# Performance work log

Measured on AMD Instinct MI355X. Metric: run time of the kernel, lower is better.

The kernel has to match this reference:

```python
import jax, jax.numpy as jnp
import numpy as np

N_NODES = 50000
N_EDGES = 400000
D = 512
LN_EPS = 1e-5


def setup_inputs() -> dict:
    key = jax.random.key(0)
    k0, k1, k2, k3 = jax.random.split(key, 4)
    x = jax.random.normal(k0, (N_NODES, D), dtype=jnp.float32)
    src = jax.random.randint(k1, (N_EDGES,), 0, N_NODES, dtype=jnp.int64)
    dst = jax.random.randint(k2, (N_EDGES,), 0, N_NODES, dtype=jnp.int64)
    W = jax.random.normal(k3, (D, D), dtype=jnp.float32) * 0.05
    b = jnp.zeros((D,), dtype=jnp.float32)
    gamma = jnp.ones((D,), dtype=jnp.float32)
    beta = jnp.zeros((D,), dtype=jnp.float32)
    return {"x": x, "W": W, "b": b, "gamma": gamma, "beta": beta, "src": src, "dst": dst}


def reference(x, W, b, gamma, beta, src, dst):
    n = x.shape[0]
    ones = jnp.ones(src.shape, dtype=x.dtype)
    # DGL GraphConv norm='both': clamp degrees to >= 1
    deg_out = jnp.clip(jax.ops.segment_sum(ones, src, num_segments=n), 1.0)  # [N]
    deg_in = jnp.clip(jax.ops.segment_sum(ones, dst, num_segments=n), 1.0)   # [N]
    h = x * jax.lax.rsqrt(deg_out)[:, None]                 # [N, D] src normalization
    agg = jax.ops.segment_sum(h[src], dst, num_segments=n)  # gather->scatter-add SpMM
    h = agg * jax.lax.rsqrt(deg_in)[:, None]                # dst normalization
    h = h @ W + b                                           # dense linear
    # LayerNorm over last dim
    mu = jnp.mean(h, axis=-1, keepdims=True)
    var = jnp.mean(jnp.square(h - mu), axis=-1, keepdims=True)
    h = (h - mu) * jax.lax.rsqrt(var + LN_EPS) * gamma + beta
    # torch nn.GELU default = exact erf GELU
    return jax.nn.gelu(h, approximate=False)
```

## Files before the change

kernel.cpp:

```cpp
#include <hip/hip_runtime.h>
#include <hip/hip_bf16.h>

#define D 512

typedef __attribute__((ext_vector_type(8))) short bf16x8;
typedef __attribute__((ext_vector_type(4))) float f32x4;

__device__ inline float b2f(short h) {
    union { unsigned u; float f; } c;
    c.u = ((unsigned)(unsigned short)h) << 16;
    return c.f;
}

__global__ void k_hist(const int* __restrict__ src, const int* __restrict__ dst,
                       int* __restrict__ deg_out, int* __restrict__ deg_in, int E) {
    int e = blockIdx.x * 256 + threadIdx.x;
    if (e < E) {
        atomicAdd(&deg_out[src[e]], 1);
        atomicAdd(&deg_in[dst[e]], 1);
    }
}

__global__ __launch_bounds__(256)
void k_scale(const float* __restrict__ x, const int* __restrict__ deg_out,
             __hip_bfloat16* __restrict__ xs, int total16) {
    int i = blockIdx.x * 256 + threadIdx.x;
    if (i >= total16) return;
    int node = i >> 6;
    float w = rsqrtf((float)max(deg_out[node], 1));
    const float4* p = (const float4*)(x + (size_t)i * 8);
    float4 a = p[0], b = p[1];
    union { float4 f4; __hip_bfloat16 h[8]; } o;
    o.h[0] = __float2bfloat16(a.x * w);
    o.h[1] = __float2bfloat16(a.y * w);
    o.h[2] = __float2bfloat16(a.z * w);
    o.h[3] = __float2bfloat16(a.w * w);
    o.h[4] = __float2bfloat16(b.x * w);
    o.h[5] = __float2bfloat16(b.y * w);
    o.h[6] = __float2bfloat16(b.z * w);
    o.h[7] = __float2bfloat16(b.w * w);
    *(float4*)(xs + (size_t)i * 8) = o.f4;
}

__global__ void k_scan1(const int* __restrict__ deg_in, int* __restrict__ row_start,
                        int* __restrict__ partials, int N) {
    __shared__ int sm[1024];
    int tid = threadIdx.x;
    int i = blockIdx.x * 1024 + tid;
    int v = (i < N) ? deg_in[i] : 0;
    sm[tid] = v;
    __syncthreads();
    int acc = v;
    #pragma unroll
    for (int off = 1; off < 1024; off <<= 1) {
        int t = (tid >= off) ? sm[tid - off] : 0;
        __syncthreads();
        acc += t;
        sm[tid] = acc;
        __syncthreads();
    }
    if (i < N) row_start[i] = acc - v;
    if (tid == 1023) partials[blockIdx.x] = acc;
}

__global__ void k_scan2w(int* __restrict__ partials, int* __restrict__ row_start,
                         int nb, int N) {
    int lane = threadIdx.x;
    int orig = (lane < nb) ? partials[lane] : 0;
    int v = orig;
    #pragma unroll
    for (int off = 1; off < 64; off <<= 1) {
        int t = __shfl_up(v, off, 64);
        if (lane >= off) v += t;
    }
    if (lane < nb) partials[lane] = v - orig;
    if (lane == 63) row_start[N] = v;
}

__global__ void k_scan2s(int* __restrict__ partials, int* __restrict__ row_start,
                         int nb, int N) {
    if (threadIdx.x == 0 && blockIdx.x == 0) {
        int run = 0;
        for (int b = 0; b < nb; b++) { int t = partials[b]; partials[b] = run; run += t; }
        row_start[N] = run;
    }
}

__global__ void k_scan3(int* __restrict__ row_start, const int* __restrict__ partials, int N) {
    int i = blockIdx.x * 256 + threadIdx.x;
    if (i < N) row_start[i] += partials[i >> 10];
}

__global__ void k_fill(const int* __restrict__ src, const int* __restrict__ dst,
                       const int* __restrict__ row_start, int* __restrict__ cursor,
                       int* __restrict__ csr_src, int E) {
    int e = blockIdx.x * 256 + threadIdx.x;
    if (e < E) {
        int d = dst[e];
        int slot = atomicAdd(&cursor[d], 1);
        csr_src[row_start[d] + slot] = src[e];
    }
}

__global__ void k_packw2(const float* __restrict__ W, __hip_bfloat16* __restrict__ Wp) {
    int bid = blockIdx.x;
    int c = bid >> 7, kt = (bid >> 3) & 15, ntc = bid & 7;
    int lane = threadIdx.x;
    int k0 = kt * 32 + (lane >> 4) * 8;
    int n  = (c * 8 + ntc) * 16 + (lane & 15);
    union { float4 f4; __hip_bfloat16 h[8]; } o;
    #pragma unroll
    for (int j = 0; j < 8; j++)
        o.h[j] = __float2bfloat16(W[(size_t)(k0 + j) * D + n]);
    *(float4*)(Wp + ((size_t)bid * 64 + lane) * 8) = o.f4;
}

__global__ __launch_bounds__(512, 2)
void k_fused(const __hip_bfloat16* __restrict__ xs, const int* __restrict__ row_start,
             const int* __restrict__ csr_src, const __hip_bfloat16* __restrict__ Wp,
             const float* __restrict__ bias, const float* __restrict__ gamma,
             const float* __restrict__ beta, float* __restrict__ out, int M) {
    __shared__ __align__(16) char ldsA[65536];
    __shared__ float s_sum[64][4];
    __shared__ float s_sq[64][4];

    int tid = threadIdx.x;
    int wid = tid >> 6, lane = tid & 63;
    int l4 = lane >> 4, coll = lane & 15;
    int tb = blockIdx.x * 64;

    {
        const __hip_bfloat16* xl = xs + (size_t)lane * 8;
        for (int i = 0; i < 8; i++) {
            int rowt = wid * 8 + i;
            int node = tb + rowt;
            char* dst = ldsA + rowt * 1024 + ((lane * 16) ^ ((rowt & 7) << 4));
            if (node < M) {
                int rs = row_start[node], re = row_start[node + 1];
                float acc[8];
                #pragma unroll
                for (int k = 0; k < 8; k++) acc[k] = 0.f;
                int j = rs;
                for (; j + 4 <= re; j += 4) {
                    int s0 = csr_src[j], s1 = csr_src[j + 1], s2 = csr_src[j + 2], s3 = csr_src[j + 3];
                    bf16x8 v0 = *(const bf16x8*)(xl + (size_t)s0 * D);
                    bf16x8 v1 = *(const bf16x8*)(xl + (size_t)s1 * D);
                    bf16x8 v2 = *(const bf16x8*)(xl + (size_t)s2 * D);
                    bf16x8 v3 = *(const bf16x8*)(xl + (size_t)s3 * D);
                    #pragma unroll
                    for (int k = 0; k < 8; k++)
                        acc[k] += (b2f(v0[k]) + b2f(v1[k])) + (b2f(v2[k]) + b2f(v3[k]));
                }
                for (; j < re; j++) {
                    int s = csr_src[j];
                    bf16x8 v = *(const bf16x8*)(xl + (size_t)s * D);
                    #pragma unroll
                    for (int k = 0; k < 8; k++) acc[k] += b2f(v[k]);
                }
                float rn = rsqrtf((float)max(re - rs, 1));
                union { float4 f4; __hip_bfloat16 h[8]; } o;
                #pragma unroll
                for (int k = 0; k < 8; k++) o.h[k] = __float2bfloat16(acc[k] * rn);
                *(float4*)dst = o.f4;
            } else {
                *(float4*)dst = (float4){0.f, 0.f, 0.f, 0.f};
            }
        }
    }
    __syncthreads();

    int wm = wid >> 2, wn = wid & 3;
    int r0 = wm * 32 + coll;
    int r1 = r0 + 16;
    const char* wb = (const char*)Wp + ((size_t)(wn * 128) * 64 + lane) * 16;

    f32x4 acc0[8], acc1[8];
    #pragma unroll
    for (int t = 0; t < 8; t++) { acc0[t] = (f32x4){0,0,0,0}; acc1[t] = (f32x4){0,0,0,0}; }

    for (int kt = 0; kt < 16; kt++) {
        int kb = kt * 64 + l4 * 16;
        bf16x8 af0 = *(const bf16x8*)(ldsA + r0 * 1024 + (kb ^ ((r0 & 7) << 4)));
        bf16x8 af1 = *(const bf16x8*)(ldsA + r1 * 1024 + (kb ^ ((r1 & 7) << 4)));
        const char* wk = wb + (size_t)kt * 8192;
        #pragma unroll
        for (int t = 0; t < 8; t++) {
            bf16x8 bf = *(const bf16x8*)(wk + (size_t)t * 1024);
            acc0[t] = __builtin_amdgcn_mfma_f32_16x16x32_bf16(af0, bf, acc0[t], 0, 0, 0);
            acc1[t] = __builtin_amdgcn_mfma_f32_16x16x32_bf16(af1, bf, acc1[t], 0, 0, 0);
        }
    }

    float bia[8], gam[8], bet[8];
    #pragma unroll
    for (int t = 0; t < 8; t++) {
        int col = wn * 128 + t * 16 + coll;
        bia[t] = bias[col]; gam[t] = gamma[col]; bet[t] = beta[col];
    }
    #pragma unroll
    for (int ai = 0; ai < 2; ai++) {
        f32x4* acc = ai ? acc1 : acc0;
        #pragma unroll
        for (int r = 0; r < 4; r++) {
            float s = 0.f, q = 0.f;
            #pragma unroll
            for (int t = 0; t < 8; t++) {
                float v = acc[t][r] + bia[t];
                acc[t][r] = v;
                s += v; q += v * v;
            }
            #pragma unroll
            for (int off = 1; off < 16; off <<= 1) {
                s += __shfl_xor(s, off, 64);
                q += __shfl_xor(q, off, 64);
            }
            if (coll == 0) {
                int rb = wm * 32 + ai * 16 + l4 * 4 + r;
                s_sum[rb][wn] = s;
                s_sq[rb][wn] = q;
            }
        }
    }
    __syncthreads();

    #pragma unroll
    for (int ai = 0; ai < 2; ai++) {
        f32x4* acc = ai ? acc1 : acc0;
        #pragma unroll
        for (int r = 0; r < 4; r++) {
            int rb = wm * 32 + ai * 16 + l4 * 4 + r;
            int gr = tb + rb;
            if (gr >= M) continue;
            float s = s_sum[rb][0] + s_sum[rb][1] + s_sum[rb][2] + s_sum[rb][3];
            float q = s_sq[rb][0] + s_sq[rb][1] + s_sq[rb][2] + s_sq[rb][3];
            float mean = s * (1.0f / 512.0f);
            float var = q * (1.0f / 512.0f) - mean * mean;
            float rstd = rsqrtf(fmaxf(var, 0.f) + 1e-5f);
            float* orow = out + (size_t)gr * D + wn * 128 + coll;
            #pragma unroll
            for (int t = 0; t < 8; t++) {
                float y = (acc[t][r] - mean) * rstd * gam[t] + bet[t];
                float yy = y * y;
                float pz = fmaf(yy, -0.1029423374f, -2.3022076728f);
                float e = __builtin_amdgcn_exp2f(y * pz);
                float g = y * __builtin_amdgcn_rcpf(1.0f + e);
                orow[t * 16] = g;
            }
        }
    }
}

__global__ __launch_bounds__(256)
void k_spmm_f32(const float* __restrict__ x, const int* __restrict__ row_start,
                const int* __restrict__ csr_src, const int* __restrict__ deg_out,
                __hip_bfloat16* __restrict__ A, int N) {
    int wid = threadIdx.x >> 6;
    int lane = threadIdx.x & 63;
    int node = blockIdx.x * 4 + wid;
    if (node >= N) return;
    int rs = row_start[node], re = row_start[node + 1];
    float4 acc0 = {0.f, 0.f, 0.f, 0.f};
    float4 acc1 = {0.f, 0.f, 0.f, 0.f};
    const float* xl = x + (size_t)lane * 8;
    for (int j = rs; j < re; j++) {
        int s = csr_src[j];
        float w = rsqrtf((float)max(deg_out[s], 1));
        const float4* p = (const float4*)(xl + (size_t)s * D);
        float4 a = p[0], b = p[1];
        acc0.x += a.x * w; acc0.y += a.y * w; acc0.z += a.z * w; acc0.w += a.w * w;
        acc1.x += b.x * w; acc1.y += b.y * w; acc1.z += b.z * w; acc1.w += b.w * w;
    }
    float rn = rsqrtf((float)max(re - rs, 1));
    union { float4 f4; __hip_bfloat16 h[8]; } o;
    o.h[0] = __float2bfloat16(acc0.x * rn);
    o.h[1] = __float2bfloat16(acc0.y * rn);
    o.h[2] = __float2bfloat16(acc0.z * rn);
    o.h[3] = __float2bfloat16(acc0.w * rn);
    o.h[4] = __float2bfloat16(acc1.x * rn);
    o.h[5] = __float2bfloat16(acc1.y * rn);
    o.h[6] = __float2bfloat16(acc1.z * rn);
    o.h[7] = __float2bfloat16(acc1.w * rn);
    *(float4*)(A + (size_t)node * D + lane * 8) = o.f4;
}

__global__ void k_packw(const float* __restrict__ W, __hip_bfloat16* __restrict__ Wp) {
    int tile = blockIdx.x;
    int lane = threadIdx.x;
    int kt = tile >> 5, nt = tile & 31;
    int k0 = kt * 32 + (lane >> 4) * 8;
    int n  = nt * 16 + (lane & 15);
    union { float4 f4; __hip_bfloat16 h[8]; } o;
    #pragma unroll
    for (int j = 0; j < 8; j++)
        o.h[j] = __float2bfloat16(W[(size_t)(k0 + j) * D + n]);
    *(float4*)(Wp + ((size_t)tile * 64 + lane) * 8) = o.f4;
}

__global__ __launch_bounds__(512)
void k_gemm(const __hip_bfloat16* __restrict__ A, const __hip_bfloat16* __restrict__ Wp,
            const float* __restrict__ bias, const float* __restrict__ gamma,
            const float* __restrict__ beta, float* __restrict__ out, int M) {
    int tid = threadIdx.x;
    int wid = tid >> 6, lane = tid & 63;
    int wm = wid >> 2;
    int wn = wid & 3;
    int l4 = lane >> 4, coll = lane & 15;
    int m0 = blockIdx.x * 32 + wm * 16;
    int arow = m0 + coll;
    bool rowok = (arow < M);

    f32x4 acc[8];
    #pragma unroll
    for (int t = 0; t < 8; t++) acc[t] = (f32x4){0.f, 0.f, 0.f, 0.f};

    const bf16x8* wpb = (const bf16x8*)Wp;
    for (int kt = 0; kt < 16; kt++) {
        bf16x8 afrag;
        if (rowok) afrag = *(const bf16x8*)(A + (size_t)arow * D + kt * 32 + l4 * 8);
        else afrag = (bf16x8){0,0,0,0,0,0,0,0};
        const bf16x8* wp = wpb + ((size_t)(kt * 32 + wn * 8) * 64 + lane);
        #pragma unroll
        for (int t = 0; t < 8; t++) {
            bf16x8 bfrag = wp[(size_t)t * 64];
            acc[t] = __builtin_amdgcn_mfma_f32_16x16x32_bf16(afrag, bfrag, acc[t], 0, 0, 0);
        }
    }
    __shared__ float s_sum[32][4];
    __shared__ float s_sq[32][4];
    #pragma unroll
    for (int r = 0; r < 4; r++) {
        float s = 0.f, q = 0.f;
        #pragma unroll
        for (int t = 0; t < 8; t++) {
            int col = wn * 128 + t * 16 + coll;
            float v = acc[t][r] + bias[col];
            acc[t][r] = v;
            s += v; q += v * v;
        }
        #pragma unroll
        for (int off = 1; off < 16; off <<= 1) {
            s += __shfl_xor(s, off, 64);
            q += __shfl_xor(q, off, 64);
        }
        if (coll == 0) {
            int rb = wm * 16 + l4 * 4 + r;
            s_sum[rb][wn] = s;
            s_sq[rb][wn] = q;
        }
    }
    __syncthreads();
    #pragma unroll
    for (int r = 0; r < 4; r++) {
        int rb = wm * 16 + l4 * 4 + r;
        int gr = blockIdx.x * 32 + rb;
        if (gr >= M) continue;
        float s = s_sum[rb][0] + s_sum[rb][1] + s_sum[rb][2] + s_sum[rb][3];
        float q = s_sq[rb][0] + s_sq[rb][1] + s_sq[rb][2] + s_sq[rb][3];
        float mean = s * (1.0f / 512.0f);
        float var = q * (1.0f / 512.0f) - mean * mean;
        float rstd = rsqrtf(fmaxf(var, 0.f) + 1e-5f);
        #pragma unroll
        for (int t = 0; t < 8; t++) {
            int col = wn * 128 + t * 16 + coll;
            float y = (acc[t][r] - mean) * rstd * gamma[col] + beta[col];
            float yy = y * y;
            float pz = fmaf(yy, -0.1029423374f, -2.3022076728f);
            float e = __builtin_amdgcn_exp2f(y * pz);
            out[(size_t)gr * D + col] = y * __builtin_amdgcn_rcpf(1.0f + e);
        }
    }
}

extern "C" void kernel_launch(void* const* d_in, const int* in_sizes, int n_in,
                              void* d_out, int out_size, void* d_ws, size_t ws_size,
                              hipStream_t stream) {
    const float* x     = (const float*)d_in[0];
    const float* W     = (const float*)d_in[1];
    const float* b     = (const float*)d_in[2];
    const float* gamma = (const float*)d_in[3];
    const float* beta  = (const float*)d_in[4];
    const int*   src   = (const int*)d_in[5];
    const int*   dst   = (const int*)d_in[6];
    int N = in_sizes[0] / D;
    int E = in_sizes[5];
    float* out = (float*)d_out;

    int* deg_out   = (int*)d_ws;
    int* deg_in    = deg_out + N;
    int* row_start = deg_in + N;
    int* cursor    = row_start + N + 1;
    int* partials  = cursor + N;
    int* csr_src   = partials + 64;
    uintptr_t p = (uintptr_t)(csr_src + E);
    p = (p + 255) & ~(uintptr_t)255;
    __hip_bfloat16* A = (__hip_bfloat16*)p;
    p += (size_t)N * D * sizeof(__hip_bfloat16);
    p = (p + 255) & ~(uintptr_t)255;
    __hip_bfloat16* Wp = (__hip_bfloat16*)p;
    p += (size_t)D * D * sizeof(__hip_bfloat16);
    p = (p + 255) & ~(uintptr_t)255;
    __hip_bfloat16* xs = (__hip_bfloat16*)p;
    size_t need_xs = (p - (uintptr_t)d_ws) + (size_t)N * D * sizeof(__hip_bfloat16);
    bool use_bf16_path = (ws_size >= need_xs);

    hipMemsetAsync(deg_out, 0, (size_t)2 * N * sizeof(int), stream);
    hipMemsetAsync(cursor, 0, (size_t)N * sizeof(int), stream);

    k_hist<<<(E + 255) / 256, 256, 0, stream>>>(src, dst, deg_out, deg_in, E);
    int nb1 = (N + 1023) / 1024;
    k_scan1<<<nb1, 1024, 0, stream>>>(deg_in, row_start, partials, N);
    if (nb1 <= 64)
        k_scan2w<<<1, 64, 0, stream>>>(partials, row_start, nb1, N);
    else
        k_scan2s<<<1, 64, 0, stream>>>(partials, row_start, nb1, N);
    k_scan3<<<(N + 255) / 256, 256, 0, stream>>>(row_start, partials, N);
    k_fill<<<(E + 255) / 256, 256, 0, stream>>>(src, dst, row_start, cursor, csr_src, E);

    if (use_bf16_path) {
        int total16 = N * 64;
        k_scale<<<(total16 + 255) / 256, 256, 0, stream>>>(x, deg_out, xs, total16);
        k_packw2<<<512, 64, 0, stream>>>(W, Wp);
        k_fused<<<(N + 63) / 64, 512, 0, stream>>>(xs, row_start, csr_src, Wp,
                                                   b, gamma, beta, out, N);
    } else {
        k_spmm_f32<<<(N + 3) / 4, 256, 0, stream>>>(x, row_start, csr_src, deg_out, A, N);
        k_packw<<<512, 64, 0, stream>>>(W, Wp);
        k_gemm<<<(N + 31) / 32, 512, 0, stream>>>(A, Wp, b, gamma, beta, out, N);
    }
}
```

Measured before the change: 291.4 us.

## Reorder to GEMM-then-aggregate: compute x·W first, gather transformed rows with fused LayerNorm/GELU

Uses linearity to apply the dense matmul before the sparse aggregation. A new GEMM kernel reads fp32 x directly, converts it to bf16 in registers, scales rows by the src-degree norm and writes a bf16 Y buffer. A gather kernel then sums neighbour rows of Y, applies the dst norm, bias, LayerNorm and GELU in one wave per node. This drops the separate scaling pass and the xs buffer, and takes the sparse gather out of the GEMM kernel, where it made the MFMA phase wait. In exchange the GEMM result is rounded to bf16 before aggregation and makes an extra round trip through memory.

```diff
diff --git a/kernel.cpp b/kernel.cpp
--- a/kernel.cpp
+++ b/kernel.cpp
@@ -19,27 +19,6 @@
         atomicAdd(&deg_out[src[e]], 1);
         atomicAdd(&deg_in[dst[e]], 1);
     }
-}
-
-__global__ __launch_bounds__(256)
-void k_scale(const float* __restrict__ x, const int* __restrict__ deg_out,
-             __hip_bfloat16* __restrict__ xs, int total16) {
-    int i = blockIdx.x * 256 + threadIdx.x;
-    if (i >= total16) return;
-    int node = i >> 6;
-    float w = rsqrtf((float)max(deg_out[node], 1));
-    const float4* p = (const float4*)(x + (size_t)i * 8);
-    float4 a = p[0], b = p[1];
-    union { float4 f4; __hip_bfloat16 h[8]; } o;
-    o.h[0] = __float2bfloat16(a.x * w);
-    o.h[1] = __float2bfloat16(a.y * w);
-    o.h[2] = __float2bfloat16(a.z * w);
-    o.h[3] = __float2bfloat16(a.w * w);
-    o.h[4] = __float2bfloat16(b.x * w);
-    o.h[5] = __float2bfloat16(b.y * w);
-    o.h[6] = __float2bfloat16(b.z * w);
-    o.h[7] = __float2bfloat16(b.w * w);
-    *(float4*)(xs + (size_t)i * 8) = o.f4;
 }
 
 __global__ void k_scan1(const int* __restrict__ deg_in, int* __restrict__ row_start,
@@ -116,62 +95,22 @@
 }
 
 __global__ __launch_bounds__(512, 2)
-void k_fused(const __hip_bfloat16* __restrict__ xs, const int* __restrict__ row_start,
-             const int* __restrict__ csr_src, const __hip_bfloat16* __restrict__ Wp,
-             const float* __restrict__ bias, const float* __restrict__ gamma,
-             const float* __restrict__ beta, float* __restrict__ out, int M) {
-    __shared__ __align__(16) char ldsA[65536];
-    __shared__ float s_sum[64][4];
-    __shared__ float s_sq[64][4];
+void k_gemmY(const float* __restrict__ x, const __hip_bfloat16* __restrict__ Wp,
+             const int* __restrict__ deg_out, __hip_bfloat16* __restrict__ y, int M) {
+    __shared__ __align__(16) char ldsY[65536];
 
     int tid = threadIdx.x;
     int wid = tid >> 6, lane = tid & 63;
+    int wm = wid >> 2, wn = wid & 3;
     int l4 = lane >> 4, coll = lane & 15;
     int tb = blockIdx.x * 64;
 
-    {
-        const __hip_bfloat16* xl = xs + (size_t)lane * 8;
-        for (int i = 0; i < 8; i++) {
-            int rowt = wid * 8 + i;
-            int node = tb + rowt;
-            char* dst = ldsA + rowt * 1024 + ((lane * 16) ^ ((rowt & 7) << 4));
-            if (node < M) {
-                int rs = row_start[node], re = row_start[node + 1];
-                float acc[8];
-                #pragma unroll
-                for (int k = 0; k < 8; k++) acc[k] = 0.f;
-                int j = rs;
-                for (; j + 4 <= re; j += 4) {
-                    int s0 = csr_src[j], s1 = csr_src[j + 1], s2 = csr_src[j + 2], s3 = csr_src[j + 3];
-                    bf16x8 v0 = *(const bf16x8*)(xl + (size_t)s0 * D);
-                    bf16x8 v1 = *(const bf16x8*)(xl + (size_t)s1 * D);
-                    bf16x8 v2 = *(const bf16x8*)(xl + (size_t)s2 * D);
-                    bf16x8 v3 = *(const bf16x8*)(xl + (size_t)s3 * D);
-                    #pragma unroll
-                    for (int k = 0; k < 8; k++)
-                        acc[k] += (b2f(v0[k]) + b2f(v1[k])) + (b2f(v2[k]) + b2f(v3[k]));
-                }
-                for (; j < re; j++) {
-                    int s = csr_src[j];
-                    bf16x8 v = *(const bf16x8*)(xl + (size_t)s * D);
-                    #pragma unroll
-                    for (int k = 0; k < 8; k++) acc[k] += b2f(v[k]);
-                }
-                float rn = rsqrtf((float)max(re - rs, 1));
-                union { float4 f4; __hip_bfloat16 h[8]; } o;
-                #pragma unroll
-                for (int k = 0; k < 8; k++) o.h[k] = __float2bfloat16(acc[k] * rn);
-                *(float4*)dst = o.f4;
-            } else {
-                *(float4*)dst = (float4){0.f, 0.f, 0.f, 0.f};
-            }
-        }
-    }
-    __syncthreads();
-
-    int wm = wid >> 2, wn = wid & 3;
     int r0 = wm * 32 + coll;
     int r1 = r0 + 16;
+    int grA = min(tb + r0, M - 1);
+    int grB = min(tb + r1, M - 1);
+    const float* xa = x + (size_t)grA * D + l4 * 8;
+    const float* xb = x + (size_t)grB * D + l4 * 8;
     const char* wb = (const char*)Wp + ((size_t)(wn * 128) * 64 + lane) * 16;
 
     f32x4 acc0[8], acc1[8];
@@ -179,75 +118,131 @@
     for (int t = 0; t < 8; t++) { acc0[t] = (f32x4){0,0,0,0}; acc1[t] = (f32x4){0,0,0,0}; }
 
     for (int kt = 0; kt < 16; kt++) {
-        int kb = kt * 64 + l4 * 16;
-        bf16x8 af0 = *(const bf16x8*)(ldsA + r0 * 1024 + (kb ^ ((r0 & 7) << 4)));
-        bf16x8 af1 = *(const bf16x8*)(ldsA + r1 * 1024 + (kb ^ ((r1 & 7) << 4)));
+        const float4* pa = (const float4*)(xa + kt * 32);
+        const float4* pb = (const float4*)(xb + kt * 32);
+        float4 a0 = pa[0], a1 = pa[1];
+        float4 b0 = pb[0], b1 = pb[1];
+        union { bf16x8 v; __hip_bfloat16 h[8]; } ua, ub;
+        ua.h[0] = __float2bfloat16(a0.x); ua.h[1] = __float2bfloat16(a0.y);
+        ua.h[2] = __float2bfloat16(a0.z); ua.h[3] = __float2bfloat16(a0.w);
+        ua.h[4] = __float2bfloat16(a1.x); ua.h[5] = __float2bfloat16(a1.y);
+        ua.h[6] = __float2bfloat16(a1.z); ua.h[7] = __float2bfloat16(a1.w);
+        ub.h[0] = __float2bfloat16(b0.x); ub.h[1] = __float2bfloat16(b0.y);
+        ub.h[2] = __float2bfloat16(b0.z); ub.h[3] = __float2bfloat16(b0.w);
+        ub.h[4] = __float2bfloat16(b1.x); ub.h[5] = __float2bfloat16(b1.y);
+        ub.h[6] = __float2bfloat16(b1.z); ub.h[7] = __float2bfloat16(b1.w);
         const char* wk = wb + (size_t)kt * 8192;
         #pragma unroll
         for (int t = 0; t < 8; t++) {
             bf16x8 bf = *(const bf16x8*)(wk + (size_t)t * 1024);
-            acc0[t] = __builtin_amdgcn_mfma_f32_16x16x32_bf16(af0, bf, acc0[t], 0, 0, 0);
-            acc1[t] = __builtin_amdgcn_mfma_f32_16x16x32_bf16(af1, bf, acc1[t], 0, 0, 0);
-        }
-    }
-
-    float bia[8], gam[8], bet[8];
-    #pragma unroll
-    for (int t = 0; t < 8; t++) {
-        int col = wn * 128 + t * 16 + coll;
-        bia[t] = bias[col]; gam[t] = gamma[col]; bet[t] = beta[col];
-    }
+            acc0[t] = __builtin_amdgcn_mfma_f32_16x16x32_bf16(ua.v, bf, acc0[t], 0, 0, 0);
+            acc1[t] = __builtin_amdgcn_mfma_f32_16x16x32_bf16(ub.v, bf, acc1[t], 0, 0, 0);
+        }
+    }
+
     #pragma unroll
     for (int ai = 0; ai < 2; ai++) {
         f32x4* acc = ai ? acc1 : acc0;
         #pragma unroll
         for (int r = 0; r < 4; r++) {
-            float s = 0.f, q = 0.f;
+            int rt = wm * 32 + ai * 16 + l4 * 4 + r;
+            int grow = min(tb + rt, M - 1);
+            float wv = rsqrtf((float)max(deg_out[grow], 1));
+            int xorv = (rt & 7) << 4;
+            char* rowp = ldsY + rt * 1024;
             #pragma unroll
             for (int t = 0; t < 8; t++) {
-                float v = acc[t][r] + bia[t];
-                acc[t][r] = v;
-                s += v; q += v * v;
+                int col = wn * 128 + t * 16 + coll;
+                *(__hip_bfloat16*)(rowp + ((col * 2) ^ xorv)) =
+                    __float2bfloat16(acc[t][r] * wv);
             }
-            #pragma unroll
-            for (int off = 1; off < 16; off <<= 1) {
-                s += __shfl_xor(s, off, 64);
-                q += __shfl_xor(q, off, 64);
-            }
-            if (coll == 0) {
-                int rb = wm * 32 + ai * 16 + l4 * 4 + r;
-                s_sum[rb][wn] = s;
-                s_sq[rb][wn] = q;
-            }
         }
     }
     __syncthreads();
 
     #pragma unroll
-    for (int ai = 0; ai < 2; ai++) {
-        f32x4* acc = ai ? acc1 : acc0;
-        #pragma unroll
-        for (int r = 0; r < 4; r++) {
-            int rb = wm * 32 + ai * 16 + l4 * 4 + r;
-            int gr = tb + rb;
-            if (gr >= M) continue;
-            float s = s_sum[rb][0] + s_sum[rb][1] + s_sum[rb][2] + s_sum[rb][3];
-            float q = s_sq[rb][0] + s_sq[rb][1] + s_sq[rb][2] + s_sq[rb][3];
-            float mean = s * (1.0f / 512.0f);
-            float var = q * (1.0f / 512.0f) - mean * mean;
-            float rstd = rsqrtf(fmaxf(var, 0.f) + 1e-5f);
-            float* orow = out + (size_t)gr * D + wn * 128 + coll;
-            #pragma unroll
-            for (int t = 0; t < 8; t++) {
-                float y = (acc[t][r] - mean) * rstd * gam[t] + bet[t];
-                float yy = y * y;
-                float pz = fmaf(yy, -0.1029423374f, -2.3022076728f);
-                float e = __builtin_amdgcn_exp2f(y * pz);
-                float g = y * __builtin_amdgcn_rcpf(1.0f + e);
-                orow[t * 16] = g;
-            }
-        }
-    }
+    for (int i = 0; i < 8; i++) {
+        int chunk = i * 512 + tid;
+        int row = chunk >> 6;
+        int cc = chunk & 63;
+        int grow = tb + row;
+        if (grow < M) {
+            float4 v = *(const float4*)(ldsY + row * 1024 + ((cc * 16) ^ ((row & 7) << 4)));
+            *(float4*)((char*)y + (size_t)grow * 1024 + cc * 16) = v;
+        }
+    }
+}
+
+__global__ __launch_bounds__(256)
+void k_gather(const __hip_bfloat16* __restrict__ y, const int* __restrict__ row_start,
+              const int* __restrict__ csr_src, const float* __restrict__ bias,
+              const float* __restrict__ gamma, const float* __restrict__ beta,
+              float* __restrict__ out, int N) {
+    int wid = threadIdx.x >> 6;
+    int lane = threadIdx.x & 63;
+    int node = blockIdx.x * 4 + wid;
+    if (node >= N) return;
+    int rs = row_start[node], re = row_start[node + 1];
+
+    float bi8[8], g8[8], b8[8];
+    #pragma unroll
+    for (int k = 0; k < 8; k++) {
+        bi8[k] = bias[lane * 8 + k];
+        g8[k] = gamma[lane * 8 + k];
+        b8[k] = beta[lane * 8 + k];
+    }
+
+    float acc[8];
+    #pragma unroll
+    for (int k = 0; k < 8; k++) acc[k] = 0.f;
+    const __hip_bfloat16* yl = y + (size_t)lane * 8;
+
+    int j = rs;
+    for (; j + 4 <= re; j += 4) {
+        int s0 = csr_src[j], s1 = csr_src[j + 1], s2 = csr_src[j + 2], s3 = csr_src[j + 3];
+        bf16x8 v0 = *(const bf16x8*)(yl + (size_t)s0 * D);
+        bf16x8 v1 = *(const bf16x8*)(yl + (size_t)s1 * D);
+        bf16x8 v2 = *(const bf16x8*)(yl + (size_t)s2 * D);
+        bf16x8 v3 = *(const bf16x8*)(yl + (size_t)s3 * D);
+        #pragma unroll
+        for (int k = 0; k < 8; k++)
+            acc[k] += (b2f(v0[k]) + b2f(v1[k])) + (b2f(v2[k]) + b2f(v3[k]));
+    }
+    for (; j < re; j++) {
+        int s = csr_src[j];
+        bf16x8 v = *(const bf16x8*)(yl + (size_t)s * D);
+        #pragma unroll
+        for (int k = 0; k < 8; k++) acc[k] += b2f(v[k]);
+    }
+
+    float rn = rsqrtf((float)max(re - rs, 1));
+    float f[8];
+    float s = 0.f, q = 0.f;
+    #pragma unroll
+    for (int k = 0; k < 8; k++) {
+        f[k] = acc[k] * rn + bi8[k];
+        s += f[k]; q += f[k] * f[k];
+    }
+    #pragma unroll
+    for (int off = 1; off < 64; off <<= 1) {
+        s += __shfl_xor(s, off, 64);
+        q += __shfl_xor(q, off, 64);
+    }
+    float mean = s * (1.0f / 512.0f);
+    float var = q * (1.0f / 512.0f) - mean * mean;
+    float rstd = rsqrtf(fmaxf(var, 0.f) + 1e-5f);
+    float o[8];
+    #pragma unroll
+    for (int k = 0; k < 8; k++) {
+        float yv = (f[k] - mean) * rstd * g8[k] + b8[k];
+        float yy = yv * yv;
+        float pz = fmaf(yy, -0.1029423374f, -2.3022076728f);
+        float e = __builtin_amdgcn_exp2f(yv * pz);
+        o[k] = yv * __builtin_amdgcn_rcpf(1.0f + e);
+    }
+    float* orow = out + (size_t)node * D + lane * 8;
+    *(float4*)orow = (float4){o[0], o[1], o[2], o[3]};
+    *(float4*)(orow + 4) = (float4){o[4], o[5], o[6], o[7]};
 }
 
 __global__ __launch_bounds__(256)
@@ -393,15 +388,12 @@
     int* csr_src   = partials + 64;
     uintptr_t p = (uintptr_t)(csr_src + E);
     p = (p + 255) & ~(uintptr_t)255;
-    __hip_bfloat16* A = (__hip_bfloat16*)p;
+    __hip_bfloat16* y = (__hip_bfloat16*)p;
     p += (size_t)N * D * sizeof(__hip_bfloat16);
     p = (p + 255) & ~(uintptr_t)255;
     __hip_bfloat16* Wp = (__hip_bfloat16*)p;
-    p += (size_t)D * D * sizeof(__hip_bfloat16);
-    p = (p + 255) & ~(uintptr_t)255;
-    __hip_bfloat16* xs = (__hip_bfloat16*)p;
-    size_t need_xs = (p - (uintptr_t)d_ws) + (size_t)N * D * sizeof(__hip_bfloat16);
-    bool use_bf16_path = (ws_size >= need_xs);
+    size_t need = (p - (uintptr_t)d_ws) + (size_t)D * D * sizeof(__hip_bfloat16);
+    bool main_path = (ws_size >= need);
 
     hipMemsetAsync(deg_out, 0, (size_t)2 * N * sizeof(int), stream);
     hipMemsetAsync(cursor, 0, (size_t)N * sizeof(int), stream);
@@ -416,15 +408,13 @@
     k_scan3<<<(N + 255) / 256, 256, 0, stream>>>(row_start, partials, N);
     k_fill<<<(E + 255) / 256, 256, 0, stream>>>(src, dst, row_start, cursor, csr_src, E);
 
-    if (use_bf16_path) {
-        int total16 = N * 64;
-        k_scale<<<(total16 + 255) / 256, 256, 0, stream>>>(x, deg_out, xs, total16);
+    if (main_path) {
         k_packw2<<<512, 64, 0, stream>>>(W, Wp);
-        k_fused<<<(N + 63) / 64, 512, 0, stream>>>(xs, row_start, csr_src, Wp,
-                                                   b, gamma, beta, out, N);
+        k_gemmY<<<(N + 63) / 64, 512, 0, stream>>>(x, Wp, deg_out, y, N);
+        k_gather<<<(N + 3) / 4, 256, 0, stream>>>(y, row_start, csr_src, b, gamma, beta, out, N);
     } else {
-        k_spmm_f32<<<(N + 3) / 4, 256, 0, stream>>>(x, row_start, csr_src, deg_out, A, N);
+        k_spmm_f32<<<(N + 3) / 4, 256, 0, stream>>>(x, row_start, csr_src, deg_out, y, N);
         k_packw<<<512, 64, 0, stream>>>(W, Wp);
-        k_gemm<<<(N + 31) / 32, 512, 0, stream>>>(A, Wp, b, gamma, beta, out, N);
-    }
-}
+        k_gemm<<<(N + 31) / 32, 512, 0, stream>>>(y, Wp, b, gamma, beta, out, N);
+    }
+}
```

Result: faster. 251.5 us (-13.7%).
